# Performance work log

Hardware: AMD Instinct MI355X
Metric: run time of the kernel (lower is better)

The kernel has to match this reference:

```python
import jax, jax.numpy as jnp
import numpy as np

N_IN = 1024
LAYER_SIZES = [2048] * 8 + [1024]  # 8 hidden layers + output layer
DEG = 32
BATCH = 1024


def setup_inputs() -> dict:
    key = jax.random.key(0)
    kx, kw, ki = jax.random.split(key, 3)
    X = jax.random.normal(kx, (BATCH, N_IN), dtype=jnp.float32)
    weight = jnp.float32(0.5)  # net.best_w, shared scalar across all nodes
    # Topologically valid children: nodes in layer l may reference any
    # previously computed node (index < offset).
    idx_blocks = []
    offset = N_IN
    for li, sz in enumerate(LAYER_SIZES):
        k = jax.random.fold_in(ki, li)
        idx_blocks.append(jax.random.randint(k, (sz, DEG), 0, offset, dtype=jnp.int32))
        offset += sz
    child_idx = jnp.concatenate(idx_blocks, axis=0)  # [sum(LAYER_SIZES), DEG]
    return {"X": X, "weight": weight, "child_idx": child_idx}


def reference(X, weight, child_idx):
    # X: [B, N_IN]; child_idx: [n_compute_nodes, DEG] (topologically ordered)
    # Each node: val = tanh(weight * sum(child_vals))  (params = w*ones(deg))
    vals = X  # input-layer node values, [B, n_nodes_so_far]
    ptr = 0
    for sz in LAYER_SIZES:
        idx = child_idx[ptr:ptr + sz]          # [sz, DEG], static slice
        ptr += sz
        gathered = vals[:, idx]                # [B, sz, DEG]
        new = jnp.tanh(weight * gathered.sum(axis=-1))  # [B, sz]
        vals = jnp.concatenate([vals, new], axis=1)
    n_out = LAYER_SIZES[-1]
    return vals[:, -n_out:]  # [B, n_outputs]
```

## Files before the change

kernel.cpp:

```cpp
#include <hip/hip_runtime.h>

#define BATCH 1024
#define N_IN 1024
#define TOTAL 18432
#define BLOCK 1024
#define NNEUR 17408

__device__ __forceinline__ float fast_tanh(float x) {
    float e = __expf(2.0f * x);
    return 1.0f - 2.0f / (1.0f + e);
}

__global__ void prep_kernel(const int4* __restrict__ cidx4, int4* __restrict__ idxT) {
    int m = blockIdx.x * blockDim.x + threadIdx.x;
    if (m >= NNEUR) return;
    int layer = min(m >> 11, 8);
    int nloc  = m - (layer << 11);
    int sz    = (layer == 8) ? 1024 : 2048;
    int ptr   = layer << 11;

    const int4* src = cidx4 + (size_t)m * 8;
    int4* dst = idxT + (size_t)ptr * 8;
    #pragma unroll
    for (int g = 0; g < 8; ++g) {
        dst[(size_t)g * sz + nloc] = src[g];
    }
}

__global__ __launch_bounds__(BLOCK) void net_kernel_t(
    const float* __restrict__ X,
    const float* __restrict__ wptr,
    const int4* __restrict__ idxT,
    float* __restrict__ out)
{
    __shared__ float2 vals[TOTAL];
    const int rowA = blockIdx.x * 2;
    const float w = wptr[0];
    const int t = threadIdx.x;

    {
        const float4* xa = reinterpret_cast<const float4*>(X + (size_t)rowA * N_IN);
        const float4* xb = reinterpret_cast<const float4*>(X + (size_t)(rowA + 1) * N_IN);
        for (int i = t; i < N_IN / 4; i += BLOCK) {
            float4 a = xa[i], b = xb[i];
            vals[4 * i + 0] = make_float2(a.x, b.x);
            vals[4 * i + 1] = make_float2(a.y, b.y);
            vals[4 * i + 2] = make_float2(a.z, b.z);
            vals[4 * i + 3] = make_float2(a.w, b.w);
        }
    }
    __syncthreads();

    int off = N_IN;
    const int4* L = idxT;
    #pragma unroll
    for (int li = 0; li < 9; ++li) {
        const int sz = (li == 8) ? 1024 : 2048;
        if (sz == 2048) {
            const int n0 = t, n1 = t + 1024;
            float a0x = 0.f, a0y = 0.f, a1x = 0.f, a1y = 0.f;
            #pragma unroll
            for (int g = 0; g < 8; ++g) {
                int4 i0 = L[(size_t)g * 2048 + n0];
                int4 i1 = L[(size_t)g * 2048 + n1];
                float2 p = vals[i0.x], q = vals[i0.y], u = vals[i0.z], s = vals[i0.w];
                a0x += (p.x + q.x) + (u.x + s.x);
                a0y += (p.y + q.y) + (u.y + s.y);
                p = vals[i1.x]; q = vals[i1.y]; u = vals[i1.z]; s = vals[i1.w];
                a1x += (p.x + q.x) + (u.x + s.x);
                a1y += (p.y + q.y) + (u.y + s.y);
            }
            vals[off + n0] = make_float2(fast_tanh(w * a0x), fast_tanh(w * a0y));
            vals[off + n1] = make_float2(fast_tanh(w * a1x), fast_tanh(w * a1y));
        } else {
            const int n0 = t;
            float a0x = 0.f, a0y = 0.f;
            #pragma unroll
            for (int g = 0; g < 8; ++g) {
                int4 i0 = L[(size_t)g * 1024 + n0];
                float2 p = vals[i0.x], q = vals[i0.y], u = vals[i0.z], s = vals[i0.w];
                a0x += (p.x + q.x) + (u.x + s.x);
                a0y += (p.y + q.y) + (u.y + s.y);
            }
            vals[off + n0] = make_float2(fast_tanh(w * a0x), fast_tanh(w * a0y));
        }
        __syncthreads();
        off += sz;
        L += (size_t)sz * 8;
    }

    {
        float* oA = out + (size_t)rowA * 1024;
        float* oB = out + (size_t)(rowA + 1) * 1024;
        const float2* src = vals + (TOTAL - 1024);
        for (int i = t; i < 1024; i += BLOCK) {
            float2 v = src[i];
            oA[i] = v.x;
            oB[i] = v.y;
        }
    }
}

__global__ __launch_bounds__(BLOCK) void net_kernel_f(
    const float* __restrict__ X,
    const float* __restrict__ wptr,
    const int* __restrict__ cidx,
    float* __restrict__ out)
{
    __shared__ float2 vals[TOTAL];
    const int rowA = blockIdx.x * 2;
    const float w = wptr[0];
    const int t = threadIdx.x;
    {
        const float4* xa = reinterpret_cast<const float4*>(X + (size_t)rowA * N_IN);
        const float4* xb = reinterpret_cast<const float4*>(X + (size_t)(rowA + 1) * N_IN);
        for (int i = t; i < N_IN / 4; i += BLOCK) {
            float4 a = xa[i], b = xb[i];
            vals[4 * i + 0] = make_float2(a.x, b.x);
            vals[4 * i + 1] = make_float2(a.y, b.y);
            vals[4 * i + 2] = make_float2(a.z, b.z);
            vals[4 * i + 3] = make_float2(a.w, b.w);
        }
    }
    __syncthreads();
    int off = N_IN, ptr = 0;
    #pragma unroll
    for (int li = 0; li < 9; ++li) {
        const int sz = (li == 8) ? 1024 : 2048;
        for (int n = t; n < sz; n += BLOCK) {
            const int4* ip = reinterpret_cast<const int4*>(cidx + (size_t)(ptr + n) * 32);
            float sx = 0.f, sy = 0.f;
            #pragma unroll
            for (int j = 0; j < 8; ++j) {
                const int4 v = ip[j];
                float2 a = vals[v.x], b = vals[v.y], c = vals[v.z], d = vals[v.w];
                sx += (a.x + b.x) + (c.x + d.x);
                sy += (a.y + b.y) + (c.y + d.y);
            }
            vals[off + n] = make_float2(fast_tanh(w * sx), fast_tanh(w * sy));
        }
        __syncthreads();
        off += sz;
        ptr += sz;
    }
    {
        float* oA = out + (size_t)rowA * 1024;
        float* oB = out + (size_t)(rowA + 1) * 1024;
        const float2* src = vals + (TOTAL - 1024);
        for (int i = t; i < 1024; i += BLOCK) {
            float2 v = src[i];
            oA[i] = v.x;
            oB[i] = v.y;
        }
    }
}

extern "C" void kernel_launch(void* const* d_in, const int* in_sizes, int n_in,
                              void* d_out, int out_size, void* d_ws, size_t ws_size,
                              hipStream_t stream)
{
    const float* X    = (const float*)d_in[0];
    const float* w    = (const float*)d_in[1];
    const int*   cidx = (const int*)d_in[2];
    float* out = (float*)d_out;

    const size_t need = (size_t)NNEUR * 32 * sizeof(int);
    if (ws_size >= need) {
        int4* idxT = (int4*)d_ws;
        hipLaunchKernelGGL(prep_kernel, dim3((NNEUR + 255) / 256), dim3(256), 0, stream,
                           (const int4*)cidx, idxT);
        hipLaunchKernelGGL(net_kernel_t, dim3(BATCH / 2), dim3(BLOCK), 0, stream,
                           X, w, idxT, out);
    } else {
        hipLaunchKernelGGL(net_kernel_f, dim3(BATCH / 2), dim3(BLOCK), 0, stream,
                           X, w, cidx, out);
    }
}
```

Before: 130.4 us.

## Reorder child indices in prep to reduce LDS bank conflicts in gathers

The prep kernel now permutes each neuron's 32 child indices into slots, so that at each gather step lanes in a wavefront tend to hit distinct LDS banks. The slot is chosen from the low index bits and the lane number, with overflow indices filling the remaining free slots. Because summation is commutative, the result is unchanged apart from float rounding order. The prep kernel gains 64KB of shared memory per block and extra per-thread work, which costs some prep time and occupancy.

```diff
diff --git a/kernel.cpp b/kernel.cpp
--- a/kernel.cpp
+++ b/kernel.cpp
@@ -11,19 +11,65 @@
     return 1.0f - 2.0f / (1.0f + e);
 }
 
-__global__ void prep_kernel(const int4* __restrict__ cidx4, int4* __restrict__ idxT) {
-    int m = blockIdx.x * blockDim.x + threadIdx.x;
+#define PREP_T 256
+__global__ __launch_bounds__(PREP_T) void prep_kernel(const int4* __restrict__ cidx4,
+                                                      int4* __restrict__ idxT) {
+    __shared__ int out_s[32 * PREP_T];
+    __shared__ int left_s[32 * PREP_T];
+    const int m = blockIdx.x * PREP_T + threadIdx.x;
+    const int tid = threadIdx.x;
     if (m >= NNEUR) return;
-    int layer = min(m >> 11, 8);
-    int nloc  = m - (layer << 11);
-    int sz    = (layer == 8) ? 1024 : 2048;
-    int ptr   = layer << 11;
+
+    const int layer = min(m >> 11, 8);
+    const int nloc  = m - (layer << 11);
+    const int sz    = (layer == 8) ? 1024 : 2048;
+    const int ptr   = layer << 11;
+    const int lane  = nloc & 63;
+    const int hiFirst = (lane & 1) << 4;
 
     const int4* src = cidx4 + (size_t)m * 8;
+    int4 v[8];
+    #pragma unroll
+    for (int g = 0; g < 8; ++g) v[g] = src[g];
+
+    unsigned slotFree = 0xFFFFFFFFu;
+    int nleft = 0;
+    #pragma unroll
+    for (int g = 0; g < 8; ++g) {
+        int comp[4] = {v[g].x, v[g].y, v[g].z, v[g].w};
+        #pragma unroll
+        for (int c = 0; c < 4; ++c) {
+            const int id = comp[c];
+            const int s1 = ((id & 15) - lane) & 15;
+            const int sA = s1 + hiFirst;
+            const int sB = s1 + (hiFirst ^ 16);
+            if (slotFree >> sA & 1u) {
+                out_s[sA * PREP_T + tid] = id;
+                slotFree &= ~(1u << sA);
+            } else if (slotFree >> sB & 1u) {
+                out_s[sB * PREP_T + tid] = id;
+                slotFree &= ~(1u << sB);
+            } else {
+                left_s[nleft * PREP_T + tid] = id;
+                ++nleft;
+            }
+        }
+    }
+    unsigned f = slotFree;
+    for (int i = 0; i < nleft; ++i) {
+        const int s = __builtin_ctz(f);
+        f &= f - 1;
+        out_s[s * PREP_T + tid] = left_s[i * PREP_T + tid];
+    }
     int4* dst = idxT + (size_t)ptr * 8;
     #pragma unroll
     for (int g = 0; g < 8; ++g) {
-        dst[(size_t)g * sz + nloc] = src[g];
+        int4 o;
+        o.x = out_s[(4 * g + 0) * PREP_T + tid];
+        o.y = out_s[(4 * g + 1) * PREP_T + tid];
+        o.z = out_s[(4 * g + 2) * PREP_T + tid];
+        o.w = out_s[(4 * g + 3) * PREP_T + tid];
+        dst[(size_t)g * sz + nloc] = o;
     }
 }
 
@@ -167,7 +213,7 @@
     const size_t need = (size_t)NNEUR * 32 * sizeof(int);
     if (ws_size >= need) {
         int4* idxT = (int4*)d_ws;
-        hipLaunchKernelGGL(prep_kernel, dim3((NNEUR + 255) / 256), dim3(256), 0, stream,
+        hipLaunchKernelGGL(prep_kernel, dim3((NNEUR + PREP_T - 1) / PREP_T), dim3(PREP_T), 0, stream,
                            (const int4*)cidx, idxT);
         hipLaunchKernelGGL(net_kernel_t, dim3(BATCH / 2), dim3(BLOCK), 0, stream,
                            X, w, idxT, out);
```

Result: faster. 126.0 us (-3.4%).
